# Kernel optimization log

Hardware: AMD Instinct MI355X
Metric: run time of the kernel (lower is better)

Reference implementation:

```python
import jax, jax.numpy as jnp
import numpy as np
from jax import lax

SAMPLING_FRACTION = 0.5
BIG = 1e8  # initial 'infinite' distance, matches torch's 1e8


def _farthest_point_sample(points, init_idx, n_sample):
    """points: (B,N,C) float; init_idx: (B,) int. Returns (B, n_sample) int32 indices."""
    B, N, C = points.shape
    batch = jnp.arange(B)

    def step(carry, _):
        distances, farthest = carry            # (B,N), (B,)
        centroid = points[batch, farthest]     # (B,C)
        d = jnp.sum((points - centroid[:, None, :]) ** 2, axis=-1)  # (B,N) squared euclid
        distances = jnp.minimum(distances, d)
        new_farthest = jnp.argmax(distances, axis=-1)
        return (distances, new_farthest), farthest  # record index BEFORE update (matches torch)

    init = (jnp.full((B, N), BIG, dtype=points.dtype), init_idx.astype(jnp.int32))
    _, centroids = lax.scan(step, init, None, length=n_sample)
    return centroids.T  # (B, n_sample)


def _index_points(x, idx):
    # x: (B, N, ...) ; idx: (B, M) -> (B, M, ...)
    return jnp.take_along_axis(x, idx.reshape(idx.shape + (1,) * (x.ndim - 2)), axis=1) if x.ndim > 2 else jnp.take_along_axis(x, idx, axis=1)


def setup_inputs() -> dict:
    key = jax.random.key(0)
    k1, k2, k3 = jax.random.split(key, 3)
    B, N, C, D = 16, 8192, 3, 256
    coords = jax.random.normal(k1, (B, N, C), dtype=jnp.float32)
    values = jax.random.normal(k2, (B, N, D), dtype=jnp.float32)
    mask = jnp.ones((B, N), dtype=jnp.float32)
    init_idx = jax.random.randint(k3, (B,), 0, N)
    return {"coords": coords, "values": values, "mask": mask, "init_idx": init_idx}


def reference(coords, values, mask, init_idx):
    B, N, C = coords.shape
    n_sample = int(round(N * SAMPLING_FRACTION))
    idx = _farthest_point_sample(coords, init_idx, n_sample)  # (B, n_sample)
    query_coords = _index_points(coords, idx)  # (B, M, C)
    query_values = _index_points(values, idx)  # (B, M, D)
    query_mask = _index_points(mask, idx)      # (B, M)
    return (query_coords, query_values, query_mask)
```

## Files before the change

kernel.cpp:

```cpp
#include <hip/hip_runtime.h>

#define FPS_N   8192
#define FPS_T   512
#define FPS_W   (FPS_T / 64)
#define FPS_PPT (FPS_N / FPS_T)
#define FPS_PR  (FPS_PPT / 2)

typedef float v2f __attribute__((ext_vector_type(2)));

__device__ __forceinline__ v2f pk_add(v2f a, v2f b) {
    v2f r; asm("v_pk_add_f32 %0, %1, %2" : "=v"(r) : "v"(a), "v"(b)); return r;
}
__device__ __forceinline__ v2f pk_mul(v2f a, v2f b) {
    v2f r; asm("v_pk_mul_f32 %0, %1, %2" : "=v"(r) : "v"(a), "v"(b)); return r;
}
__device__ __forceinline__ v2f pk_fma(v2f a, v2f b, v2f c) {
    v2f r; asm("v_pk_fma_f32 %0, %1, %2, %3" : "=v"(r) : "v"(a), "v"(b), "v"(c)); return r;
}

template<int CTRL>
__device__ __forceinline__ float dpp_max_step(float x) {
    int s = __builtin_amdgcn_update_dpp(0, __float_as_int(x), CTRL, 0xf, 0xf, true);
    return fmaxf(x, __int_as_float(s));
}

__device__ __forceinline__ float wave_max_nn(float x) {
    x = dpp_max_step<0x111>(x);
    x = dpp_max_step<0x112>(x);
    x = dpp_max_step<0x114>(x);
    x = dpp_max_step<0x118>(x);
    x = dpp_max_step<0x142>(x);
    x = dpp_max_step<0x143>(x);
    return __int_as_float(__builtin_amdgcn_readlane(__float_as_int(x), 63));
}

__device__ __forceinline__ float readlane_f(float x, int l) {
    return __int_as_float(__builtin_amdgcn_readlane(__float_as_int(x), l));
}

__global__ __launch_bounds__(FPS_T) void fps_kernel(
    const float* __restrict__ coords,
    const int*   __restrict__ init_idx,
    int*         __restrict__ out_idx,
    int M)
{
    __shared__ float sx[FPS_N], sy[FPS_N], sz[FPS_N];
    __shared__ float swd[2][FPS_W];
    __shared__ int   swi[2][FPS_W];
    __shared__ float scx[2][FPS_W], scy[2][FPS_W], scz[2][FPS_W];

    const int b    = blockIdx.x;
    const int tid  = threadIdx.x;
    const int lane = tid & 63;
    const int wv   = tid >> 6;
    const float* cb = coords + (size_t)b * FPS_N * 3;

    float f[48];
    const float4* cb4 = reinterpret_cast<const float4*>(cb);
    #pragma unroll
    for (int i = 0; i < 12; ++i) {
        float4 v = cb4[tid * 12 + i];
        f[i * 4 + 0] = v.x; f[i * 4 + 1] = v.y;
        f[i * 4 + 2] = v.z; f[i * 4 + 3] = v.w;
    }

    v2f px[FPS_PR], py[FPS_PR], pz[FPS_PR], dist[FPS_PR];
    const int base = tid * FPS_PPT;
    #pragma unroll
    for (int k = 0; k < FPS_PPT; ++k) {
        sx[base + k] = f[3 * k + 0];
        sy[base + k] = f[3 * k + 1];
        sz[base + k] = f[3 * k + 2];
    }
    #pragma unroll
    for (int j = 0; j < FPS_PR; ++j) {
        px[j] = v2f{f[6 * j + 0], f[6 * j + 3]};
        py[j] = v2f{f[6 * j + 1], f[6 * j + 4]};
        pz[j] = v2f{f[6 * j + 2], f[6 * j + 5]};
        dist[j] = v2f{1e8f, 1e8f};
    }
    __syncthreads();

    int far = init_idx[b];
    float cx = sx[far], cy = sy[far], cz = sz[far];

    for (int s = 0; s < M; ++s) {
        if (tid == 0) out_idx[b * M + s] = far;

        const v2f ncx = v2f{-cx, -cx};
        const v2f ncy = v2f{-cy, -cy};
        const v2f ncz = v2f{-cz, -cz};
        float m = 0.0f;
        #pragma unroll
        for (int j = 0; j < FPS_PR; ++j) {
            v2f dx2 = pk_add(px[j], ncx);
            v2f dy2 = pk_add(py[j], ncy);
            v2f dz2 = pk_add(pz[j], ncz);
            v2f d2  = pk_fma(dz2, dz2, pk_fma(dy2, dy2, pk_mul(dx2, dx2)));
            v2f nd;
            nd.x = fminf(dist[j].x, d2.x);
            nd.y = fminf(dist[j].y, d2.y);
            dist[j] = nd;
            m = fmaxf(m, fmaxf(nd.x, nd.y));
        }
        int myidx = base;
        #pragma unroll
        for (int j = FPS_PR - 1; j >= 0; --j) {
            myidx = (dist[j].y == m) ? base + 2 * j + 1 : myidx;
            myidx = (dist[j].x == m) ? base + 2 * j     : myidx;
        }

        float wm = wave_max_nn(m);
        unsigned long long ball = __ballot(m == wm);
        int fl   = (int)__builtin_ctzll(ball);
        int widx = __builtin_amdgcn_readlane(myidx, fl);

        const int par = s & 1;
        if (lane == 0) {
            float wcx = sx[widx], wcy = sy[widx], wcz = sz[widx];
            swd[par][wv] = wm;  swi[par][wv] = widx;
            scx[par][wv] = wcx; scy[par][wv] = wcy; scz[par][wv] = wcz;
        }
        __syncthreads();

        float dval = 0.0f, cxl = 0.0f, cyl = 0.0f, czl = 0.0f;
        int   idxl = 0;
        if (lane < FPS_W) {
            dval = swd[par][lane]; idxl = swi[par][lane];
            cxl  = scx[par][lane]; cyl = scy[par][lane]; czl = scz[par][lane];
        }
        float g = dval;
        g = dpp_max_step<0x111>(g);
        g = dpp_max_step<0x112>(g);
        g = dpp_max_step<0x114>(g);
        float gm = readlane_f(g, 7);
        unsigned long long b2 = __ballot(lane < FPS_W && dval == gm);
        int w2 = (int)__builtin_ctzll(b2);
        far = __builtin_amdgcn_readlane(idxl, w2);
        cx  = readlane_f(cxl, w2);
        cy  = readlane_f(cyl, w2);
        cz  = readlane_f(czl, w2);
    }
}

__global__ void gather_kernel(
    const float* __restrict__ coords,
    const float* __restrict__ values,
    const float* __restrict__ mask,
    const int*   __restrict__ idx,
    float* __restrict__ out_coords,
    float* __restrict__ out_values,
    float* __restrict__ out_mask,
    int N, int M, int D)
{
    const int bm = blockIdx.x;
    const int b  = bm / M;
    const int m  = bm - b * M;
    const int j  = idx[bm];
    const int l  = threadIdx.x;

    const float4* src = reinterpret_cast<const float4*>(values + ((size_t)b * N + j) * D);
    float4*       dst = reinterpret_cast<float4*>(out_values + ((size_t)b * M + m) * D);
    dst[l] = src[l];

    if (l < 3) {
        out_coords[((size_t)b * M + m) * 3 + l] = coords[((size_t)b * N + j) * 3 + l];
    } else if (l == 3) {
        out_mask[(size_t)b * M + m] = mask[(size_t)b * N + j];
    }
}

extern "C" void kernel_launch(void* const* d_in, const int* in_sizes, int n_in,
                              void* d_out, int out_size, void* d_ws, size_t ws_size,
                              hipStream_t stream)
{
    const float* coords   = (const float*)d_in[0];
    const float* values   = (const float*)d_in[1];
    const float* mask     = (const float*)d_in[2];
    const int*   init_idx = (const int*)d_in[3];

    const int B = in_sizes[3];
    const int N = in_sizes[2] / B;
    const int D = in_sizes[1] / (B * N);
    const int M = N / 2;

    float* out_coords = (float*)d_out;
    float* out_values = out_coords + (size_t)B * M * 3;
    float* out_mask   = out_values + (size_t)B * M * D;

    int* idx = (int*)d_ws;

    fps_kernel<<<B, FPS_T, 0, stream>>>(coords, init_idx, idx, M);
    gather_kernel<<<B * M, D / 4, 0, stream>>>(coords, values, mask, idx,
                                               out_coords, out_values, out_mask,
                                               N, M, D);
}
```

Measured before the change: 3.792 ms.

## Split each batch's FPS across 8 cooperating blocks with global-memory atomic handshakes

Each batch's farthest-point search now runs on 8 blocks of 256 threads instead of one block of 512, so 128 blocks share the GPU instead of 16. Each block holds a full copy of the coordinates in LDS but computes distances only for its slice. Every iteration, each wave publishes its max distance, index and iteration tag as a packed 64-bit value in global memory, then spins until all 32 wave slots for the batch are tagged before reducing. This trades the block-local barrier for inter-block spin waits, which adds global-memory latency per step. It relies on all 8 blocks of a batch being resident together, or it can deadlock.

```diff
diff --git a/kernel.cpp b/kernel.cpp
--- a/kernel.cpp
+++ b/kernel.cpp
@@ -1,12 +1,15 @@
 #include <hip/hip_runtime.h>
 
+typedef unsigned long long u64;
+typedef float v2f __attribute__((ext_vector_type(2)));
+
 #define FPS_N   8192
-#define FPS_T   512
+#define FPS_G   8
+#define FPS_T   256
 #define FPS_W   (FPS_T / 64)
-#define FPS_PPT (FPS_N / FPS_T)
+#define FPS_SL  (FPS_G * FPS_W)
+#define FPS_PPT (FPS_N / FPS_G / FPS_T)
 #define FPS_PR  (FPS_PPT / 2)
-
-typedef float v2f __attribute__((ext_vector_type(2)));
 
 __device__ __forceinline__ v2f pk_add(v2f a, v2f b) {
     v2f r; asm("v_pk_add_f32 %0, %1, %2" : "=v"(r) : "v"(a), "v"(b)); return r;
@@ -23,7 +26,6 @@
     int s = __builtin_amdgcn_update_dpp(0, __float_as_int(x), CTRL, 0xf, 0xf, true);
     return fmaxf(x, __int_as_float(s));
 }
-
 __device__ __forceinline__ float wave_max_nn(float x) {
     x = dpp_max_step<0x111>(x);
     x = dpp_max_step<0x112>(x);
@@ -34,58 +36,58 @@
     return __int_as_float(__builtin_amdgcn_readlane(__float_as_int(x), 63));
 }
 
-__device__ __forceinline__ float readlane_f(float x, int l) {
-    return __int_as_float(__builtin_amdgcn_readlane(__float_as_int(x), l));
+__global__ void zero_sync(u64* __restrict__ sync, int n) {
+    int i = blockIdx.x * blockDim.x + threadIdx.x;
+    if (i < n) sync[i] = 0ull;
 }
 
 __global__ __launch_bounds__(FPS_T) void fps_kernel(
     const float* __restrict__ coords,
     const int*   __restrict__ init_idx,
     int*         __restrict__ out_idx,
+    u64*         __restrict__ sync,
     int M)
 {
     __shared__ float sx[FPS_N], sy[FPS_N], sz[FPS_N];
-    __shared__ float swd[2][FPS_W];
-    __shared__ int   swi[2][FPS_W];
-    __shared__ float scx[2][FPS_W], scy[2][FPS_W], scz[2][FPS_W];
-
-    const int b    = blockIdx.x;
+
+    const int blk  = blockIdx.x;
+    const int b    = blk / FPS_G;
+    const int g    = blk - b * FPS_G;
     const int tid  = threadIdx.x;
     const int lane = tid & 63;
     const int wv   = tid >> 6;
-    const float* cb = coords + (size_t)b * FPS_N * 3;
-
-    float f[48];
-    const float4* cb4 = reinterpret_cast<const float4*>(cb);
+    const int slot_id = g * FPS_W + wv;
+    u64* syncb = sync + (size_t)b * 2 * FPS_SL;
+
+    const float4* cb4 = reinterpret_cast<const float4*>(coords + (size_t)b * FPS_N * 3);
+    float f[96];
     #pragma unroll
-    for (int i = 0; i < 12; ++i) {
-        float4 v = cb4[tid * 12 + i];
-        f[i * 4 + 0] = v.x; f[i * 4 + 1] = v.y;
-        f[i * 4 + 2] = v.z; f[i * 4 + 3] = v.w;
-    }
-
+    for (int i = 0; i < 24; ++i) {
+        float4 v = cb4[tid * 24 + i];
+        f[i*4+0] = v.x; f[i*4+1] = v.y; f[i*4+2] = v.z; f[i*4+3] = v.w;
+    }
+    const int sbase = tid * 32;
+    #pragma unroll
+    for (int k = 0; k < 32; ++k) {
+        sx[sbase+k] = f[3*k+0]; sy[sbase+k] = f[3*k+1]; sz[sbase+k] = f[3*k+2];
+    }
+    __syncthreads();
+
+    const int base = g * (FPS_N / FPS_G) + tid * FPS_PPT;
     v2f px[FPS_PR], py[FPS_PR], pz[FPS_PR], dist[FPS_PR];
-    const int base = tid * FPS_PPT;
-    #pragma unroll
-    for (int k = 0; k < FPS_PPT; ++k) {
-        sx[base + k] = f[3 * k + 0];
-        sy[base + k] = f[3 * k + 1];
-        sz[base + k] = f[3 * k + 2];
-    }
     #pragma unroll
     for (int j = 0; j < FPS_PR; ++j) {
-        px[j] = v2f{f[6 * j + 0], f[6 * j + 3]};
-        py[j] = v2f{f[6 * j + 1], f[6 * j + 4]};
-        pz[j] = v2f{f[6 * j + 2], f[6 * j + 5]};
+        px[j] = v2f{sx[base+2*j], sx[base+2*j+1]};
+        py[j] = v2f{sy[base+2*j], sy[base+2*j+1]};
+        pz[j] = v2f{sz[base+2*j], sz[base+2*j+1]};
         dist[j] = v2f{1e8f, 1e8f};
     }
-    __syncthreads();
 
     int far = init_idx[b];
     float cx = sx[far], cy = sy[far], cz = sz[far];
 
     for (int s = 0; s < M; ++s) {
-        if (tid == 0) out_idx[b * M + s] = far;
+        if (g == 0 && tid == 0) out_idx[b * M + s] = far;
 
         const v2f ncx = v2f{-cx, -cx};
         const v2f ncy = v2f{-cy, -cy};
@@ -106,40 +108,38 @@
         int myidx = base;
         #pragma unroll
         for (int j = FPS_PR - 1; j >= 0; --j) {
-            myidx = (dist[j].y == m) ? base + 2 * j + 1 : myidx;
-            myidx = (dist[j].x == m) ? base + 2 * j     : myidx;
+            myidx = (dist[j].y == m) ? base + 2*j + 1 : myidx;
+            myidx = (dist[j].x == m) ? base + 2*j     : myidx;
         }
 
         float wm = wave_max_nn(m);
-        unsigned long long ball = __ballot(m == wm);
+        u64 ball = __ballot(m == wm);
         int fl   = (int)__builtin_ctzll(ball);
         int widx = __builtin_amdgcn_readlane(myidx, fl);
 
         const int par = s & 1;
         if (lane == 0) {
-            float wcx = sx[widx], wcy = sy[widx], wcz = sz[widx];
-            swd[par][wv] = wm;  swi[par][wv] = widx;
-            scx[par][wv] = wcx; scy[par][wv] = wcy; scz[par][wv] = wcz;
+            u64 pk = ((u64)(unsigned)__float_as_uint(wm) << 32)
+                   | ((u64)(unsigned)widx << 13)
+                   | (u64)(unsigned)(s + 1);
+            __hip_atomic_store(&syncb[par * FPS_SL + slot_id], pk,
+                               __ATOMIC_RELAXED, __HIP_MEMORY_SCOPE_AGENT);
         }
-        __syncthreads();
-
-        float dval = 0.0f, cxl = 0.0f, cyl = 0.0f, czl = 0.0f;
-        int   idxl = 0;
-        if (lane < FPS_W) {
-            dval = swd[par][lane]; idxl = swi[par][lane];
-            cxl  = scx[par][lane]; cyl = scy[par][lane]; czl = scz[par][lane];
-        }
-        float g = dval;
-        g = dpp_max_step<0x111>(g);
-        g = dpp_max_step<0x112>(g);
-        g = dpp_max_step<0x114>(g);
-        float gm = readlane_f(g, 7);
-        unsigned long long b2 = __ballot(lane < FPS_W && dval == gm);
-        int w2 = (int)__builtin_ctzll(b2);
-        far = __builtin_amdgcn_readlane(idxl, w2);
-        cx  = readlane_f(cxl, w2);
-        cy  = readlane_f(cyl, w2);
-        cz  = readlane_f(czl, w2);
+
+        u64* pslot = &syncb[par * FPS_SL + (lane & (FPS_SL - 1))];
+        const unsigned tag = (unsigned)(s + 1);
+        u64 v;
+        do {
+            v = __hip_atomic_load(pslot, __ATOMIC_RELAXED, __HIP_MEMORY_SCOPE_AGENT);
+        } while (!__all((unsigned)(v & 0x1FFFull) == tag));
+
+        float cand = __int_as_float((int)(v >> 32));
+        int   cidx = (int)((v >> 13) & 0x1FFF);
+        float gm = wave_max_nn(cand);
+        u64 b2 = __ballot(cand == gm);
+        int l2 = (int)__builtin_ctzll(b2);
+        far = __builtin_amdgcn_readlane(cidx, l2);
+        cx = sx[far]; cy = sy[far]; cz = sz[far];
     }
 }
 
@@ -188,9 +188,12 @@
     float* out_values = out_coords + (size_t)B * M * 3;
     float* out_mask   = out_values + (size_t)B * M * D;
 
-    int* idx = (int*)d_ws;
-
-    fps_kernel<<<B, FPS_T, 0, stream>>>(coords, init_idx, idx, M);
+    int* idx  = (int*)d_ws;
+    u64* sync = (u64*)((char*)d_ws + (size_t)B * M * sizeof(int));
+    const int nsync = B * 2 * FPS_SL;
+
+    zero_sync<<<(nsync + 255) / 256, 256, 0, stream>>>(sync, nsync);
+    fps_kernel<<<B * FPS_G, FPS_T, 0, stream>>>(coords, init_idx, idx, sync, M);
     gather_kernel<<<B * M, D / 4, 0, stream>>>(coords, values, mask, idx,
                                                out_coords, out_values, out_mask,
                                                N, M, D);
```

Result: slower. 8.840 ms (+133.1%).
